# Kernel optimization log

Measured on AMD Instinct MI355X. Metric: run time of the kernel, lower is better.

Reference implementation:

```python
import jax, jax.numpy as jnp
import numpy as np

S, D = 16384, 1024


def setup_inputs() -> dict:
    key = jax.random.key(0)
    ks = jax.random.split(key, 7)
    stdv = 1.0 / np.sqrt(D)
    u = lambda k, shape: jax.random.uniform(k, shape, jnp.float32, -stdv, stdv)
    return {
        "x": jax.random.normal(ks[0], (S, D), jnp.float32),
        "Wq": u(ks[1], (D, D)), "bq": u(ks[2], (D,)),
        "Wk": u(ks[3], (D, D)), "bk": u(ks[4], (D,)),
        "Wv": u(ks[5], (D, D)), "bv": u(ks[6], (D,)),
    }


def reference(x, Wq, bq, Wk, bk, Wv, bv):
    # torch.nn.Linear: y = x @ W^T + b
    q = x @ Wq.T + bq          # [S, D]
    k = x @ Wk.T + bk          # [S, D]
    v = x @ Wv.T + bv          # [S, D]
    d = x.shape[-1]
    # NOTE: faithful to source -- scores are over the FEATURE axis: [D, D]
    scores = jnp.einsum('sd,se->de', q, k) / jnp.sqrt(jnp.float32(d))
    attn = jax.nn.softmax(scores, axis=-1)   # [D, D]
    out = v @ attn                           # [S, D]
    return out, attn
```

## Files before the change

### kernel.cpp

```cpp
#include <hip/hip_runtime.h>
#include <hip/hip_bf16.h>
#include <stdint.h>


#define S_ 16384
#define D_ 1024

typedef _Float16 half8 __attribute__((ext_vector_type(8)));
typedef _Float16 half4 __attribute__((ext_vector_type(4)));
typedef float f32x4 __attribute__((ext_vector_type(4)));

__device__ __forceinline__ void gload_lds16(const _Float16* g, _Float16* l) {
    __builtin_amdgcn_global_load_lds(
        (const __attribute__((address_space(1))) void*)g,
        (__attribute__((address_space(3))) void*)l, 16, 0, 0);
}

#define VM8() do { asm volatile("s_waitcnt vmcnt(8)" ::: "memory"); __builtin_amdgcn_sched_barrier(0); } while (0)
#define VM0() do { asm volatile("s_waitcnt vmcnt(0)" ::: "memory"); __builtin_amdgcn_sched_barrier(0); } while (0)
#define BAR() __builtin_amdgcn_s_barrier()
#define LGKM0() do { asm volatile("s_waitcnt lgkmcnt(0)" ::: "memory"); __builtin_amdgcn_sched_barrier(0); } while (0)
#define LGKM8() do { asm volatile("s_waitcnt lgkmcnt(8)" ::: "memory"); __builtin_amdgcn_sched_barrier(0); } while (0)
#define PRIO1() __builtin_amdgcn_s_setprio(1)
#define PRIO0() __builtin_amdgcn_s_setprio(0)

#define PAIR10(PI, BY, BX) do { \
    if ((PI) < 4) { BY = 0; BX = (PI); } \
    else if ((PI) < 7) { BY = 1; BX = (PI) - 3; } \
    else if ((PI) < 9) { BY = 2; BX = (PI) - 5; } \
    else { BY = 3; BX = 3; } \
} while (0)

#define STAGEA(H, KT, NX) do { \
    const _Float16* _s = srcA + (size_t)((H) * 128) * 16384 + (size_t)(KT) * 64; \
    _Float16* _d = AsS + (NX) * 16384 + ((H) * 128 + 8 * w) * 64; \
    gload_lds16(_s, _d); \
    gload_lds16(_s + (size_t)64 * 16384, _d + 4096); \
} while (0)

#define STAGEB(H, KT, NX) do { \
    const _Float16* _s = srcB + (size_t)((H) * 128) * 16384 + (size_t)(KT) * 64; \
    _Float16* _d = BsS + (NX) * 16384 + ((H) * 128 + 8 * w) * 64; \
    gload_lds16(_s, _d); \
    gload_lds16(_s + (size_t)64 * 16384, _d + 4096); \
} while (0)

#define READA(PA, QA) do { _Pragma("unroll") \
    for (int fm = 0; fm < 4; ++fm) { \
        af[fm][0] = *(const half8*)((PA) + (((QA) * 128 + fm * 16) << 7) + cx0); \
        af[fm][1] = *(const half8*)((PA) + (((QA) * 128 + fm * 16) << 7) + cx1); } \
} while (0)

#define READB(PB, BF, QB) do { _Pragma("unroll") \
    for (int fn = 0; fn < 2; ++fn) { \
        BF[fn][0] = *(const half8*)((PB) + (((QB) * 128 + fn * 16) << 7) + cx0); \
        BF[fn][1] = *(const half8*)((PB) + (((QB) * 128 + fn * 16) << 7) + cx1); } \
} while (0)

#define MFMAB(QA, QB, BF) do { _Pragma("unroll") \
    for (int fm = 0; fm < 4; ++fm) { _Pragma("unroll") \
        for (int fn = 0; fn < 2; ++fn) { \
            f32x4 _c = acc[(QA) * 4 + fm][(QB) * 2 + fn]; \
            _c = __builtin_amdgcn_mfma_f32_16x16x32_f16(af[fm][0], BF[fn][0], _c, 0, 0, 0); \
            _c = __builtin_amdgcn_mfma_f32_16x16x32_f16(af[fm][1], BF[fn][1], _c, 0, 0, 0); \
            acc[(QA) * 4 + fm][(QB) * 2 + fn] = _c; } } \
} while (0)

__global__ __launch_bounds__(512, 2)
void gemm256G(const _Float16* __restrict__ A, _Float16* __restrict__ C) {
    __shared__ _Float16 SM2[65536];
    _Float16* AsS = SM2;
    _Float16* BsS = SM2 + 32768;
    const int t = threadIdx.x;
    const int l = t & 63;
    const int w = t >> 6;
    const int wm = w >> 2, wn = w & 3;

    const int hb = blockIdx.x;
    const int lg = (hb & 7) * 20 + (hb >> 3);
    const int bz = lg / 10;
    const int pi = lg - bz * 10;
    int by, bx;
    PAIR10(pi, by, bx);
    const size_t m0 = (size_t)by * 256;
    const size_t n0 = (size_t)bx * 256;
    const size_t k0 = (size_t)bz * 1024;
    const long long coff = (long long)bz * 1048576LL;

    const int colsw = 8 * ((l & 7) ^ (l >> 3));
    const _Float16* srcA = A + (m0 + 8 * w + (l >> 3)) * (size_t)16384 + k0 + colsw;
    const _Float16* srcB = A + (n0 + 8 * w + (l >> 3)) * (size_t)16384 + k0 + colsw;

    const int cx0 = (((l >> 4) << 4)) ^ ((l & 7) << 4);
    const int cx1 = (64 + ((l >> 4) << 4)) ^ ((l & 7) << 4);
    const char* basePA = (const char*)AsS + ((wm * 64 + (l & 15)) << 7);
    const char* basePB = (const char*)BsS + ((wn * 32 + (l & 15)) << 7);

    f32x4 acc[8][4] = {};
    half8 af[4][2], bf0[2][2], bf1[2][2];

    const int nk = 16;

    STAGEA(0, 0, 0); STAGEB(0, 0, 0); STAGEB(1, 0, 0); STAGEA(1, 0, 0);
    STAGEA(0, 1, 1); STAGEB(0, 1, 1); STAGEB(1, 1, 1); STAGEA(1, 1, 1);

    for (int kt = 0; kt < nk; ++kt) {
        const int p = kt & 1;
        const int ks = kt + 2;
        const bool hs = ks < nk;
        const char* pA = basePA + p * 32768;
        const char* pB = basePB + p * 32768;

        if (kt == nk - 1) VM0(); else VM8();
        BAR();

        READA(pA, 0); READB(pB, bf0, 0);
        LGKM8();
        BAR(); LGKM0();
        PRIO1(); MFMAB(0, 0, bf0); PRIO0(); BAR();

        READB(pB, bf1, 1);
        if (hs) { STAGEA(0, ks, p); STAGEB(0, ks, p); }
        BAR(); LGKM0();
        PRIO1(); MFMAB(0, 1, bf1); PRIO0(); BAR();

        READA(pA, 1);
        if (hs) STAGEB(1, ks, p);
        BAR(); LGKM0();
        PRIO1(); MFMAB(1, 1, bf1); PRIO0(); BAR();

        if (hs) STAGEA(1, ks, p);
        PRIO1(); MFMAB(1, 0, bf0); PRIO0(); BAR();
    }

    _Float16* eb = SM2;
    const int cr = (l >> 4) << 2;
    const int cc = l & 15;
#pragma unroll
    for (int h = 0; h < 2; ++h) {
        BAR();
#pragma unroll
        for (int mm = 0; mm < 4; ++mm) {
#pragma unroll
            for (int n = 0; n < 4; ++n) {
                const int lrow0 = wm * 64 + mm * 16 + cr;
                const int lcol = (n >> 1) * 128 + wn * 32 + (n & 1) * 16 + cc;
#pragma unroll
                for (int r = 0; r < 4; ++r)
                    eb[(lrow0 + r) * 264 + lcol] = (_Float16)acc[h * 4 + mm][n][r];
            }
        }
        LGKM0();
        BAR();
#pragma unroll
        for (int i = 0; i < 8; ++i) {
            const int lrow = w * 16 + i * 2 + (l >> 5);
            const half8 v = *(const half8*)(eb + lrow * 264 + (l & 31) * 8);
            const size_t row = m0 + (size_t)h * 128 + lrow;
            const size_t col = n0 + (l & 31) * 8;
            __builtin_nontemporal_store(v,
                (half8*)(C + coff + (long long)row * 1024 + col));
        }
        LGKM0();
    }
}

__global__ __launch_bounds__(256)
void reduce_h_u(const _Float16* __restrict__ part, _Float16* __restrict__ G16) {
    const int b = blockIdx.x;
    const int ti = b >> 5;
    int by, bx;
    PAIR10(ti, by, bx);
    const int e0 = (b & 31) * 2048 + threadIdx.x * 8;
    const size_t row = (size_t)by * 256 + (e0 >> 8);
    const size_t col = (size_t)bx * 256 + (e0 & 255);
    const size_t off = row * 1024 + col;
    float s[8] = {};
    for (int z = 0; z < 16; ++z) {
        half8 v = *(const half8*)(part + (size_t)z * 1048576 + off);
#pragma unroll
        for (int j = 0; j < 8; ++j) s[j] += (float)v[j];
    }
    half8 o;
#pragma unroll
    for (int j = 0; j < 8; ++j) o[j] = (_Float16)s[j];
    *(half8*)(G16 + off) = o;
}

__global__ __launch_bounds__(256)
void mirror_g(_Float16* __restrict__ G) {
    __shared__ _Float16 tile[64][66];
    const int p = blockIdx.y;
    int by, bx;
    if (p < 3) { by = 0; bx = p + 1; }
    else if (p < 5) { by = 1; bx = p - 1; }
    else { by = 2; bx = 3; }
    const int sy = blockIdx.x >> 2, sx = blockIdx.x & 3;
    const int r0 = by * 256 + sy * 64;
    const int c0 = bx * 256 + sx * 64;
    const int t = threadIdx.x;
    const int cg = t & 15;
    const int rb = t >> 4;
#pragma unroll
    for (int it = 0; it < 4; ++it) {
        const int rr = rb + it * 16;
        half4 v = *(const half4*)(G + (size_t)(r0 + rr) * 1024 + c0 + cg * 4);
        tile[rr][cg * 4 + 0] = v[0]; tile[rr][cg * 4 + 1] = v[1];
        tile[rr][cg * 4 + 2] = v[2]; tile[rr][cg * 4 + 3] = v[3];
    }
    __syncthreads();
    const int i = t >> 2, ch = (t & 3) * 16;
    half8 h0v, h1v;
#pragma unroll
    for (int j = 0; j < 8; ++j) h0v[j] = tile[ch + j][i];
#pragma unroll
    for (int j = 0; j < 8; ++j) h1v[j] = tile[ch + 8 + j][i];
    *(half8*)(G + (size_t)(c0 + i) * 1024 + r0 + ch) = h0v;
    *(half8*)(G + (size_t)(c0 + i) * 1024 + r0 + ch + 8) = h1v;
}

#define STG128(SRC, LD, DST, KT) do { \
    const _Float16* _s = (SRC) + (size_t)(KT) * 64; \
    _Float16* _d = (DST) + 8 * w * 64; \
    gload_lds16(_s, _d); \
    gload_lds16(_s + (size_t)32 * (LD), _d + 2048); \
    gload_lds16(_s + (size_t)64 * (LD), _d + 4096); \
    gload_lds16(_s + (size_t)96 * (LD), _d + 6144); \
} while (0)

__global__ __launch_bounds__(256, 2)
void gemm128(const _Float16* __restrict__ A, const _Float16* __restrict__ B,
             float* __restrict__ C, const float* __restrict__ bias,
             int lda, int ldb, int ldc, int ksub,
             int ntx, int cpx) {
    __shared__ _Float16 SM[32768];
    const int t = threadIdx.x;
    const int l = t & 63;
    const int w = t >> 6;
    const int wm = w >> 1, wn = w & 1;

    const int hb = blockIdx.x;
    const int lg = (hb & 7) * cpx + (hb >> 3);
    const int by = lg / ntx;
    const int bx = lg - by * ntx;
    const size_t m0 = (size_t)by * 128;
    const size_t n0 = (size_t)bx * 128;

    const int colsw = 8 * ((l & 7) ^ (l >> 3));
    const _Float16* srcA = A + (m0 + 8 * w + (l >> 3)) * (size_t)lda + colsw;
    const _Float16* srcB = B + (n0 + 8 * w + (l >> 3)) * (size_t)ldb + colsw;

    const int cx0 = (((l >> 4) << 4)) ^ ((l & 7) << 4);
    const int cx1 = (64 + ((l >> 4) << 4)) ^ ((l & 7) << 4);
    const char* basePA = (const char*)SM + ((wm * 64 + (l & 15)) << 7);
    const char* basePB = (const char*)SM + 32768 + ((wn * 64 + (l & 15)) << 7);

    f32x4 acc[4][4] = {};
    half8 af[4][2], bf[4][2];

    const int nk = ksub >> 6;

    STG128(srcA, lda, SM + 0, 0);        STG128(srcB, ldb, SM + 16384, 0);
    STG128(srcA, lda, SM + 8192, 1);     STG128(srcB, ldb, SM + 24576, 1);

    for (int kt = 0; kt < nk; ++kt) {
        const int p = kt & 1;
        const int ks = kt + 2;
        const bool hs = ks < nk;
        const char* pA = basePA + p * 16384;
        const char* pB = basePB + p * 16384;

        if (kt == nk - 1) VM0(); else VM8();
        BAR();

#pragma unroll
        for (int fm = 0; fm < 4; ++fm) {
            af[fm][0] = *(const half8*)(pA + ((fm * 16) << 7) + cx0);
            af[fm][1] = *(const half8*)(pA + ((fm * 16) << 7) + cx1);
        }
#pragma unroll
        for (int fn = 0; fn < 4; ++fn) {
            bf[fn][0] = *(const half8*)(pB + ((fn * 16) << 7) + cx0);
            bf[fn][1] = *(const half8*)(pB + ((fn * 16) << 7) + cx1);
        }
        LGKM0();
        PRIO1();
#pragma unroll
        for (int fm = 0; fm < 4; ++fm)
#pragma unroll
            for (int fn = 0; fn < 4; ++fn)
                acc[fm][fn] = __builtin_amdgcn_mfma_f32_16x16x32_f16(af[fm][0], bf[fn][0], acc[fm][fn], 0, 0, 0);
        PRIO0();
        BAR();

        if (hs) {
            STG128(srcA, lda, SM + p * 8192, ks);
            STG128(srcB, ldb, SM + 16384 + p * 8192, ks);
        }
        PRIO1();
#pragma unroll
        for (int fm = 0; fm < 4; ++fm)
#pragma unroll
            for (int fn = 0; fn < 4; ++fn)
                acc[fm][fn] = __builtin_amdgcn_mfma_f32_16x16x32_f16(af[fm][1], bf[fn][1], acc[fm][fn], 0, 0, 0);
        PRIO0();
        BAR();
    }

    float* lw = (float*)((char*)SM + w * 16384);
    const int cr = (l >> 4) << 2;
    const int cc = l & 15;
    float bb4[4];
#pragma unroll
    for (int fn = 0; fn < 4; ++fn)
        bb4[fn] = bias[n0 + wn * 64 + fn * 16 + cc];
#pragma unroll
    for (int h = 0; h < 2; ++h) {
#pragma unroll
        for (int mm2 = 0; mm2 < 2; ++mm2) {
            const int mm = h * 2 + mm2;
#pragma unroll
            for (int fn = 0; fn < 4; ++fn) {
                const int lcol = fn * 16 + cc;
                const int lrow = mm2 * 16 + cr;
#pragma unroll
                for (int r = 0; r < 4; ++r)
                    lw[(lrow + r) * 68 + lcol] = acc[mm][fn][r] + bb4[fn];
            }
        }
        LGKM0();
        const size_t grow0 = m0 + (size_t)wm * 64 + h * 32;
#pragma unroll
        for (int i = 0; i < 8; ++i) {
            const int lrow = i * 4 + (l >> 4);
            const int lcol = (l & 15) * 4;
            const f32x4 v = *(const f32x4*)(lw + lrow * 68 + lcol);
            __builtin_nontemporal_store(v,
                (f32x4*)(C + (size_t)(grow0 + lrow) * ldc + n0 + wn * 64 + lcol));
        }
        LGKM0();
    }
}

template <int F16OUT>
__global__ __launch_bounds__(256, 2)
void gemm_s128(const _Float16* __restrict__ A, const _Float16* __restrict__ B,
               void* __restrict__ C, int lda, int ldb, int ldc, int ksub,
               long long mn) {
    __shared__ _Float16 SM[32768];
    const int t = threadIdx.x;
    const int l = t & 63;
    const int w = t >> 6;
    const int wm = w >> 1, wn = w & 1;

    const size_t m0 = (size_t)blockIdx.y * 128;
    const size_t n0 = (size_t)blockIdx.x * 128;
    const size_t k0 = (size_t)blockIdx.z * (size_t)ksub;
    const long long coff = (long long)blockIdx.z * mn;

    const int colsw = 8 * ((l & 7) ^ (l >> 3));
    const _Float16* srcA = A + (m0 + 8 * w + (l >> 3)) * (size_t)lda + k0 + colsw;
    const _Float16* srcB = B + (n0 + 8 * w + (l >> 3)) * (size_t)ldb + k0 + colsw;

    const int cx0 = (((l >> 4) << 4)) ^ ((l & 7) << 4);
    const int cx1 = (64 + ((l >> 4) << 4)) ^ ((l & 7) << 4);
    const char* basePA = (const char*)SM + ((wm * 64 + (l & 15)) << 7);
    const char* basePB = (const char*)SM + 32768 + ((wn * 64 + (l & 15)) << 7);

    f32x4 acc[4][4] = {};
    half8 af[4][2], bf[4][2];

    const int nk = ksub >> 6;

    STG128(srcA, lda, SM + 0, 0);        STG128(srcB, ldb, SM + 16384, 0);
    STG128(srcA, lda, SM + 8192, 1);     STG128(srcB, ldb, SM + 24576, 1);

    for (int kt = 0; kt < nk; ++kt) {
        const int p = kt & 1;
        const int ks = kt + 2;
        const bool hs = ks < nk;
        const char* pA = basePA + p * 16384;
        const char* pB = basePB + p * 16384;

        if (kt == nk - 1) VM0(); else VM8();
        BAR();

#pragma unroll
        for (int fm = 0; fm < 4; ++fm) {
            af[fm][0] = *(const half8*)(pA + ((fm * 16) << 7) + cx0);
            af[fm][1] = *(const half8*)(pA + ((fm * 16) << 7) + cx1);
        }
#pragma unroll
        for (int fn = 0; fn < 4; ++fn) {
            bf[fn][0] = *(const half8*)(pB + ((fn * 16) << 7) + cx0);
            bf[fn][1] = *(const half8*)(pB + ((fn * 16) << 7) + cx1);
        }
        LGKM0();
        PRIO1();
#pragma unroll
        for (int fm = 0; fm < 4; ++fm)
#pragma unroll
            for (int fn = 0; fn < 4; ++fn)
                acc[fm][fn] = __builtin_amdgcn_mfma_f32_16x16x32_f16(af[fm][0], bf[fn][0], acc[fm][fn], 0, 0, 0);
        PRIO0();
        BAR();

        if (hs) {
            STG128(srcA, lda, SM + p * 8192, ks);
            STG128(srcB, ldb, SM + 16384 + p * 8192, ks);
        }
        PRIO1();
#pragma unroll
        for (int fm = 0; fm < 4; ++fm)
#pragma unroll
            for (int fn = 0; fn < 4; ++fn)
                acc[fm][fn] = __builtin_amdgcn_mfma_f32_16x16x32_f16(af[fm][1], bf[fn][1], acc[fm][fn], 0, 0, 0);
        PRIO0();
        BAR();
    }

    const int cr = (l >> 4) << 2;
    const int cc = l & 15;

    if (F16OUT) {
        _Float16* eb = SM;
#pragma unroll
        for (int fm = 0; fm < 4; ++fm) {
#pragma unroll
            for (int fn = 0; fn < 4; ++fn) {
                const int lrow0 = wm * 64 + fm * 16 + cr;
                const int lcol = wn * 64 + fn * 16 + cc;
#pragma unroll
                for (int r = 0; r < 4; ++r)
                    eb[(lrow0 + r) * 132 + lcol] = (_Float16)acc[fm][fn][r];
            }
        }
        LGKM0();
        BAR();
        _Float16* Ch = (_Float16*)C;
#pragma unroll
        for (int i = 0; i < 8; ++i) {
            const int row = i * 16 + (t >> 4);
            const int colh = (t & 15) * 8;
            const half8 v = *(const half8*)(eb + row * 132 + colh);
            *(half8*)(Ch + coff + (long long)(m0 + row) * ldc + n0 + colh) = v;
        }
    } else {
        float* lw = (float*)((char*)SM + w * 16384);
        float* Cf = (float*)C;
#pragma unroll
        for (int h = 0; h < 2; ++h) {
#pragma unroll
            for (int mm2 = 0; mm2 < 2; ++mm2) {
                const int mm = h * 2 + mm2;
#pragma unroll
                for (int fn = 0; fn < 4; ++fn) {
                    const int lcol = fn * 16 + cc;
                    const int lrow = mm2 * 16 + cr;
#pragma unroll
                    for (int r = 0; r < 4; ++r)
                        lw[(lrow + r) * 68 + lcol] = acc[mm][fn][r];
                }
            }
            LGKM0();
            const size_t grow0 = m0 + (size_t)wm * 64 + h * 32;
#pragma unroll
            for (int i = 0; i < 8; ++i) {
                const int lrow = i * 4 + (l >> 4);
                const int lcol = (l & 15) * 4;
                const f32x4 v = *(const f32x4*)(lw + lrow * 68 + lcol);
                *(f32x4*)(Cf + coff + (long long)(grow0 + lrow) * ldc + n0 + wn * 64 + lcol) = v;
            }
            LGKM0();
        }
    }
}

template <int WRITE_ROW, int COLSUM>
__global__ __launch_bounds__(256)
void cast_transpose(const float* __restrict__ in, _Float16* __restrict__ outRow,
                    _Float16* __restrict__ outT, float* __restrict__ msum, int ldT) {
    __shared__ _Float16 tile[64][66];
    __shared__ float red[16][16][4];
    const int t = threadIdx.x;
    const int c0 = blockIdx.x * 64;
    const int r0 = blockIdx.y * 64;
    const int cg = t & 15;
    const int rb = t >> 4;
    f32x4 csum = {};
#pragma unroll
    for (int it = 0; it < 4; ++it) {
        const int rr = rb + it * 16;
        f32x4 v = *(const f32x4*)(in + (size_t)(r0 + rr) * 1024 + c0 + cg * 4);
        if (COLSUM) { csum[0] += v[0]; csum[1] += v[1]; csum[2] += v[2]; csum[3] += v[3]; }
        _Float16 h0 = (_Float16)v[0], h1 = (_Float16)v[1];
        _Float16 h2 = (_Float16)v[2], h3 = (_Float16)v[3];
        tile[rr][cg * 4 + 0] = h0; tile[rr][cg * 4 + 1] = h1;
        tile[rr][cg * 4 + 2] = h2; tile[rr][cg * 4 + 3] = h3;
        if (WRITE_ROW) {
            half4 h = {h0, h1, h2, h3};
            *(half4*)(outRow + (size_t)(r0 + rr) * 1024 + c0 + cg * 4) = h;
        }
    }
    if (COLSUM) {
        red[rb][cg][0] = csum[0]; red[rb][cg][1] = csum[1];
        red[rb][cg][2] = csum[2]; red[rb][cg][3] = csum[3];
    }
    __syncthreads();
    if (COLSUM && t < 64) {
        float s = 0.f;
#pragma unroll
        for (int k = 0; k < 16; ++k) s += red[k][t >> 2][t & 3];
        atomicAdd(msum + c0 + t, s);
    }
    const int i = t >> 2, ch = (t & 3) * 16;
    half8 h0v, h1v;
#pragma unroll
    for (int j = 0; j < 8; ++j) h0v[j] = tile[ch + j][i];
#pragma unroll
    for (int j = 0; j < 8; ++j) h1v[j] = tile[ch + 8 + j][i];
    *(half8*)(outT + (size_t)(c0 + i) * ldT + r0 + ch) = h0v;
    *(half8*)(outT + (size_t)(c0 + i) * ldT + r0 + ch + 8) = h1v;
}

__global__ __launch_bounds__(256)
void prep_w(const float* __restrict__ Wq, const float* __restrict__ Wk,
            const float* __restrict__ Wv, const float* __restrict__ bq,
            const float* __restrict__ m,
            _Float16* __restrict__ wq16, _Float16* __restrict__ wk16,
            _Float16* __restrict__ wvT16,
            float* __restrict__ u2, float* __restrict__ w) {
    __shared__ _Float16 tile[64][66];
    __shared__ float wred[4];
    const int b = blockIdx.x;
    const int t = threadIdx.x;

    if (b < 1024) {
        const bool isQ = b < 512;
        const int bb = isQ ? b : b - 512;
        const float* W = isQ ? Wq : Wk;
        _Float16* o = isQ ? wq16 : wk16;
        const size_t base = (size_t)bb * 2048 + (size_t)t * 8;
        const f32x4* p = (const f32x4*)(W + base);
        f32x4 x0 = p[0], x1 = p[1];
        half8 h;
        h[0] = (_Float16)x0[0]; h[1] = (_Float16)x0[1];
        h[2] = (_Float16)x0[2]; h[3] = (_Float16)x0[3];
        h[4] = (_Float16)x1[0]; h[5] = (_Float16)x1[1];
        h[6] = (_Float16)x1[2]; h[7] = (_Float16)x1[3];
        ((half8*)o)[bb * 256 + t] = h;
        const int col = (t * 8) & 1023;
        f32x4 m0 = *(const f32x4*)(m + col);
        f32x4 m1 = *(const f32x4*)(m + col + 4);
        float s = x0[0] * m0[0] + x0[1] * m0[1] + x0[2] * m0[2] + x0[3] * m0[3]
                + x1[0] * m1[0] + x1[1] * m1[1] + x1[2] * m1[2] + x1[3] * m1[3];
        for (int o2 = 32; o2; o2 >>= 1) s += __shfl_xor(s, o2);
        if ((t & 63) == 0) wred[t >> 6] = s;
        __syncthreads();
        if (t == 0) {
            const int rA = 2 * bb, rB = 2 * bb + 1;
            const float vA = wred[0] + wred[1];
            const float vB = wred[2] + wred[3];
            if (isQ) {
                u2[rA] = vA + 16384.0f * bq[rA];
                u2[rB] = vB + 16384.0f * bq[rB];
            } else {
                w[rA] = vA;
                w[rB] = vB;
            }
        }
        return;
    }

    const int bb = b - 1024;
    const int c0 = (bb & 15) * 64;
    const int r0 = (bb >> 4) * 64;
    const int cg = t & 15;
    const int rb = t >> 4;
#pragma unroll
    for (int it = 0; it < 4; ++it) {
        const int rr = rb + it * 16;
        f32x4 v = *(const f32x4*)(Wv + (size_t)(r0 + rr) * 1024 + c0 + cg * 4);
        tile[rr][cg * 4 + 0] = (_Float16)v[0];
        tile[rr][cg * 4 + 1] = (_Float16)v[1];
        tile[rr][cg * 4 + 2] = (_Float16)v[2];
        tile[rr][cg * 4 + 3] = (_Float16)v[3];
    }
    __syncthreads();
    const int i = t >> 2, ch = (t & 3) * 16;
    half8 h0v, h1v;
#pragma unroll
    for (int j = 0; j < 8; ++j) h0v[j] = tile[ch + j][i];
#pragma unroll
    for (int j = 0; j < 8; ++j) h1v[j] = tile[ch + 8 + j][i];
    *(half8*)(wvT16 + (size_t)(c0 + i) * 1024 + r0 + ch) = h0v;
    *(half8*)(wvT16 + (size_t)(c0 + i) * 1024 + r0 + ch + 8) = h1v;
}

__global__ void zero_vec(float* __restrict__ p, int n) {
    int i = blockIdx.x * 256 + threadIdx.x;
    if (i < n) p[i] = 0.f;
}

__global__ __launch_bounds__(256)
void reduce_h(const _Float16* __restrict__ part, _Float16* __restrict__ outh,
              int nz) {
    const size_t off = ((size_t)blockIdx.x * 256 + threadIdx.x) * 8;
    float s[8] = {};
    for (int z = 0; z < nz; ++z) {
        half8 v = *(const half8*)(part + (size_t)z * 1048576 + off);
#pragma unroll
        for (int j = 0; j < 8; ++j) s[j] += (float)v[j];
    }
    half8 o;
#pragma unroll
    for (int j = 0; j < 8; ++j) o[j] = (_Float16)s[j];
    *(half8*)(outh + off) = o;
}

__global__ __launch_bounds__(256)
void softmax_rows(const float* __restrict__ part, const float* __restrict__ u2,
                  const float* __restrict__ bq, const float* __restrict__ bk,
                  const float* __restrict__ w,
                  float* __restrict__ P, _Float16* __restrict__ PT) {
    const int a = blockIdx.x;
    const int t = threadIdx.x;
    __shared__ float red[8];
    const size_t off = (size_t)a * 1024 + t * 4;
    f32x4 s = {};
#pragma unroll
    for (int z = 0; z < 4; ++z) {
        f32x4 v = *(const f32x4*)(part + (size_t)z * 1048576 + off);
        s[0] += v[0]; s[1] += v[1]; s[2] += v[2]; s[3] += v[3];
    }
    const float ru = u2[a], rb = bq[a];
    f32x4 bk4 = *(const f32x4*)(bk + t * 4);
    f32x4 w4 = *(const f32x4*)(w + t * 4);
#pragma unroll
    for (int j = 0; j < 4; ++j) s[j] = (s[j] + ru * bk4[j] + rb * w4[j]) * 0.03125f;

    float m = fmaxf(fmaxf(s[0], s[1]), fmaxf(s[2], s[3]));
    for (int o = 32; o; o >>= 1) m = fmaxf(m, __shfl_xor(m, o));
    if ((t & 63) == 0) red[t >> 6] = m;
    __syncthreads();
    m = fmaxf(fmaxf(red[0], red[1]), fmaxf(red[2], red[3]));

    float e0 = expf(s[0] - m), e1 = expf(s[1] - m);
    float e2 = expf(s[2] - m), e3 = expf(s[3] - m);
    float sum = e0 + e1 + e2 + e3;
    for (int o = 32; o; o >>= 1) sum += __shfl_xor(sum, o);
    if ((t & 63) == 0) red[4 + (t >> 6)] = sum;
    __syncthreads();
    sum = red[4] + red[5] + red[6] + red[7];
    const float inv = 1.0f / sum;

    f32x4 o4 = {e0 * inv, e1 * inv, e2 * inv, e3 * inv};
    *(f32x4*)(P + off) = o4;
    const int b = t * 4;
    PT[(size_t)(b + 0) * 1024 + a] = (_Float16)o4[0];
    PT[(size_t)(b + 1) * 1024 + a] = (_Float16)o4[1];
    PT[(size_t)(b + 2) * 1024 + a] = (_Float16)o4[2];
    PT[(size_t)(b + 3) * 1024 + a] = (_Float16)o4[3];
}

__global__ __launch_bounds__(256)
void attn_bv(const float* __restrict__ attn, const float* __restrict__ bv,
             float* __restrict__ c) {
    const int j = blockIdx.x * 256 + threadIdx.x;
    const int a0 = blockIdx.y * 64;
    float s = 0.f;
#pragma unroll 4
    for (int k = 0; k < 64; ++k) {
        const int a = a0 + k;
        s += attn[(size_t)a * 1024 + j] * bv[a];
    }
    atomicAdd(c + j, s);
}

extern "C" void kernel_launch(void* const* d_in, const int* in_sizes, int n_in,
                              void* d_out, int out_size, void* d_ws, size_t ws_size,
                              hipStream_t stream) {
    const float* x  = (const float*)d_in[0];
    const float* Wq = (const float*)d_in[1];
    const float* bq = (const float*)d_in[2];
    const float* Wk = (const float*)d_in[3];
    const float* bk = (const float*)d_in[4];
    const float* Wv = (const float*)d_in[5];
    const float* bv = (const float*)d_in[6];
    float* out  = (float*)d_out;
    float* attn = out + (size_t)S_ * D_;

    char* ws = (char*)d_ws;
    float*    part  = (float*)ws;
    _Float16* partH = (_Float16*)ws;
    _Float16* x16   = (_Float16*)(ws + 33554432);
    _Float16* xT16  = (_Float16*)(ws + 67108864);
    _Float16* wq16  = (_Float16*)(ws + 100663296);
    _Float16* wk16  = (_Float16*)(ws + 102760448);
    _Float16* wvT16 = (_Float16*)(ws + 104857600);
    _Float16* G16   = (_Float16*)(ws + 106954752);
    _Float16* U16   = (_Float16*)(ws + 109051904);
    _Float16* PT    = (_Float16*)(ws + 111149056);
    _Float16* MT16  = (_Float16*)(ws + 113246208);
    float*    mvec  = (float*)(ws + 115343360);
    float*    u2    = mvec + 1024;
    float*    wv    = u2 + 1024;
    float*    cvec  = wv + 1024;

    zero_vec<<<16, 256, 0, stream>>>(mvec, 4096);
    cast_transpose<1, 1><<<dim3(16, 256), 256, 0, stream>>>(x, x16, xT16, mvec, S_);
    prep_w<<<1280, 256, 0, stream>>>(Wq, Wk, Wv, bq, mvec,
                                     wq16, wk16, wvT16, u2, wv);

    gemm256G<<<160, 512, 0, stream>>>(xT16, partH);
    reduce_h_u<<<320, 256, 0, stream>>>(partH, G16);
    mirror_g<<<dim3(16, 6), 256, 0, stream>>>(G16);
    gemm_s128<1><<<dim3(8, 8, 4), 256, 0, stream>>>(wq16, G16, (void*)partH,
                                                    1024, 1024, 1024, 256, 1048576);
    reduce_h<<<512, 256, 0, stream>>>(partH, U16, 4);
    gemm_s128<0><<<dim3(8, 8, 4), 256, 0, stream>>>(U16, wk16, (void*)part,
                                                    1024, 1024, 1024, 256, 1048576);
    softmax_rows<<<1024, 256, 0, stream>>>(part, u2, bq, bk, wv, attn, PT);
    attn_bv<<<dim3(4, 16), 256, 0, stream>>>(attn, bv, cvec);
    gemm_s128<1><<<dim3(8, 8, 4), 256, 0, stream>>>(PT, wvT16, (void*)partH,
                                                    1024, 1024, 1024, 256, 1048576);
    reduce_h<<<512, 256, 0, stream>>>(partH, MT16, 4);
    gemm128<<<1024, 256, 0, stream>>>(x16, MT16, out, cvec,
                                      1024, 1024, 1024, 1024, 8, 128);
}
```

Baseline: 165.5 us.

## Fuse weight prep into Gram GEMM, mirror in reduce, bias-vec into MT GEMM

Weight casting and transposing now run as extra blocks inside the Gram GEMM launch instead of as a separate prep kernel. The Gram reduction writes the mirrored transpose of off-diagonal tiles itself, which removes the mirror_g kernel. The attn·bv vector reduction now runs as extra blocks of a dedicated PT×WvT GEMM kernel. Together these cut three kernel launches and the serial gaps between them, at the cost of mixed-role blocks competing for CUs and the heavier 512-thread LDS footprint being applied to the lightweight prep blocks.

New measurement: 154.9 us, median of 2. 1.07x faster.

```diff
diff --git a/kernel.cpp b/kernel.cpp
--- a/kernel.cpp
+++ b/kernel.cpp
@@ -67,111 +67,197 @@
 } while (0)
 
 __global__ __launch_bounds__(512, 2)
-void gemm256G(const _Float16* __restrict__ A, _Float16* __restrict__ C) {
+void g_and_prep(const _Float16* __restrict__ A, _Float16* __restrict__ C,
+                const float* __restrict__ Wq, const float* __restrict__ Wk,
+                const float* __restrict__ Wv, const float* __restrict__ bq,
+                const float* __restrict__ m,
+                _Float16* __restrict__ wq16, _Float16* __restrict__ wk16,
+                _Float16* __restrict__ wvT16,
+                float* __restrict__ u2, float* __restrict__ wvec) {
     __shared__ _Float16 SM2[65536];
-    _Float16* AsS = SM2;
-    _Float16* BsS = SM2 + 32768;
     const int t = threadIdx.x;
-    const int l = t & 63;
-    const int w = t >> 6;
-    const int wm = w >> 2, wn = w & 3;
-
-    const int hb = blockIdx.x;
-    const int lg = (hb & 7) * 20 + (hb >> 3);
-    const int bz = lg / 10;
-    const int pi = lg - bz * 10;
-    int by, bx;
-    PAIR10(pi, by, bx);
-    const size_t m0 = (size_t)by * 256;
-    const size_t n0 = (size_t)bx * 256;
-    const size_t k0 = (size_t)bz * 1024;
-    const long long coff = (long long)bz * 1048576LL;
-
-    const int colsw = 8 * ((l & 7) ^ (l >> 3));
-    const _Float16* srcA = A + (m0 + 8 * w + (l >> 3)) * (size_t)16384 + k0 + colsw;
-    const _Float16* srcB = A + (n0 + 8 * w + (l >> 3)) * (size_t)16384 + k0 + colsw;
-
-    const int cx0 = (((l >> 4) << 4)) ^ ((l & 7) << 4);
-    const int cx1 = (64 + ((l >> 4) << 4)) ^ ((l & 7) << 4);
-    const char* basePA = (const char*)AsS + ((wm * 64 + (l & 15)) << 7);
-    const char* basePB = (const char*)BsS + ((wn * 32 + (l & 15)) << 7);
-
-    f32x4 acc[8][4] = {};
-    half8 af[4][2], bf0[2][2], bf1[2][2];
-
-    const int nk = 16;
-
-    STAGEA(0, 0, 0); STAGEB(0, 0, 0); STAGEB(1, 0, 0); STAGEA(1, 0, 0);
-    STAGEA(0, 1, 1); STAGEB(0, 1, 1); STAGEB(1, 1, 1); STAGEA(1, 1, 1);
-
-    for (int kt = 0; kt < nk; ++kt) {
-        const int p = kt & 1;
-        const int ks = kt + 2;
-        const bool hs = ks < nk;
-        const char* pA = basePA + p * 32768;
-        const char* pB = basePB + p * 32768;
-
-        if (kt == nk - 1) VM0(); else VM8();
-        BAR();
-
-        READA(pA, 0); READB(pB, bf0, 0);
-        LGKM8();
-        BAR(); LGKM0();
-        PRIO1(); MFMAB(0, 0, bf0); PRIO0(); BAR();
-
-        READB(pB, bf1, 1);
-        if (hs) { STAGEA(0, ks, p); STAGEB(0, ks, p); }
-        BAR(); LGKM0();
-        PRIO1(); MFMAB(0, 1, bf1); PRIO0(); BAR();
-
-        READA(pA, 1);
-        if (hs) STAGEB(1, ks, p);
-        BAR(); LGKM0();
-        PRIO1(); MFMAB(1, 1, bf1); PRIO0(); BAR();
-
-        if (hs) STAGEA(1, ks, p);
-        PRIO1(); MFMAB(1, 0, bf0); PRIO0(); BAR();
-    }
-
-    _Float16* eb = SM2;
-    const int cr = (l >> 4) << 2;
-    const int cc = l & 15;
-#pragma unroll
-    for (int h = 0; h < 2; ++h) {
-        BAR();
-#pragma unroll
-        for (int mm = 0; mm < 4; ++mm) {
-#pragma unroll
-            for (int n = 0; n < 4; ++n) {
-                const int lrow0 = wm * 64 + mm * 16 + cr;
-                const int lcol = (n >> 1) * 128 + wn * 32 + (n & 1) * 16 + cc;
-#pragma unroll
-                for (int r = 0; r < 4; ++r)
-                    eb[(lrow0 + r) * 264 + lcol] = (_Float16)acc[h * 4 + mm][n][r];
+
+    if (blockIdx.x < 160) {
+        _Float16* AsS = SM2;
+        _Float16* BsS = SM2 + 32768;
+        const int l = t & 63;
+        const int w = t >> 6;
+        const int wm = w >> 2, wn = w & 3;
+
+        const int hb = blockIdx.x;
+        const int lg = (hb & 7) * 20 + (hb >> 3);
+        const int bz = lg / 10;
+        const int pi = lg - bz * 10;
+        int by, bx;
+        PAIR10(pi, by, bx);
+        const size_t m0 = (size_t)by * 256;
+        const size_t n0 = (size_t)bx * 256;
+        const size_t k0 = (size_t)bz * 1024;
+        const long long coff = (long long)bz * 1048576LL;
+
+        const int colsw = 8 * ((l & 7) ^ (l >> 3));
+        const _Float16* srcA = A + (m0 + 8 * w + (l >> 3)) * (size_t)16384 + k0 + colsw;
+        const _Float16* srcB = A + (n0 + 8 * w + (l >> 3)) * (size_t)16384 + k0 + colsw;
+
+        const int cx0 = (((l >> 4) << 4)) ^ ((l & 7) << 4);
+        const int cx1 = (64 + ((l >> 4) << 4)) ^ ((l & 7) << 4);
+        const char* basePA = (const char*)AsS + ((wm * 64 + (l & 15)) << 7);
+        const char* basePB = (const char*)BsS + ((wn * 32 + (l & 15)) << 7);
+
+        f32x4 acc[8][4] = {};
+        half8 af[4][2], bf0[2][2], bf1[2][2];
+
+        const int nk = 16;
+
+        STAGEA(0, 0, 0); STAGEB(0, 0, 0); STAGEB(1, 0, 0); STAGEA(1, 0, 0);
+        STAGEA(0, 1, 1); STAGEB(0, 1, 1); STAGEB(1, 1, 1); STAGEA(1, 1, 1);
+
+        for (int kt = 0; kt < nk; ++kt) {
+            const int p = kt & 1;
+            const int ks = kt + 2;
+            const bool hs = ks < nk;
+            const char* pA = basePA + p * 32768;
+            const char* pB = basePB + p * 32768;
+
+            if (kt == nk - 1) VM0(); else VM8();
+            BAR();
+
+            READA(pA, 0); READB(pB, bf0, 0);
+            LGKM8();
+            BAR(); LGKM0();
+            PRIO1(); MFMAB(0, 0, bf0); PRIO0(); BAR();
+
+            READB(pB, bf1, 1);
+            if (hs) { STAGEA(0, ks, p); STAGEB(0, ks, p); }
+            BAR(); LGKM0();
+            PRIO1(); MFMAB(0, 1, bf1); PRIO0(); BAR();
+
+            READA(pA, 1);
+            if (hs) STAGEB(1, ks, p);
+            BAR(); LGKM0();
+            PRIO1(); MFMAB(1, 1, bf1); PRIO0(); BAR();
+
+            if (hs) STAGEA(1, ks, p);
+            PRIO1(); MFMAB(1, 0, bf0); PRIO0(); BAR();
+        }
+
+        _Float16* eb = SM2;
+        const int cr = (l >> 4) << 2;
+        const int cc = l & 15;
+#pragma unroll
+        for (int h = 0; h < 2; ++h) {
+            BAR();
+#pragma unroll
+            for (int mm = 0; mm < 4; ++mm) {
+#pragma unroll
+                for (int n = 0; n < 4; ++n) {
+                    const int lrow0 = wm * 64 + mm * 16 + cr;
+                    const int lcol = (n >> 1) * 128 + wn * 32 + (n & 1) * 16 + cc;
+#pragma unroll
+                    for (int r = 0; r < 4; ++r)
+                        eb[(lrow0 + r) * 264 + lcol] = (_Float16)acc[h * 4 + mm][n][r];
+                }
             }
-        }
-        LGKM0();
-        BAR();
-#pragma unroll
-        for (int i = 0; i < 8; ++i) {
-            const int lrow = w * 16 + i * 2 + (l >> 5);
-            const half8 v = *(const half8*)(eb + lrow * 264 + (l & 31) * 8);
-            const size_t row = m0 + (size_t)h * 128 + lrow;
-            const size_t col = n0 + (l & 31) * 8;
-            __builtin_nontemporal_store(v,
-                (half8*)(C + coff + (long long)row * 1024 + col));
-        }
-        LGKM0();
+            LGKM0();
+            BAR();
+#pragma unroll
+            for (int i = 0; i < 8; ++i) {
+                const int lrow = w * 16 + i * 2 + (l >> 5);
+                const half8 v = *(const half8*)(eb + lrow * 264 + (l & 31) * 8);
+                const size_t row = m0 + (size_t)h * 128 + lrow;
+                const size_t col = n0 + (l & 31) * 8;
+                __builtin_nontemporal_store(v,
+                    (half8*)(C + coff + (long long)row * 1024 + col));
+            }
+            LGKM0();
+        }
+        return;
+    }
+
+    const int h = t >> 8;
+    const int vt = t & 255;
+    const int vb = (blockIdx.x - 160) * 2 + h;
+    _Float16* tileh = SM2 + h * 4224;
+    float* wredAll = (float*)(SM2 + 16896);
+    const bool isW = vb < 1024;
+
+    if (isW) {
+        const bool isQ = vb < 512;
+        const int bb = isQ ? vb : vb - 512;
+        const float* W = isQ ? Wq : Wk;
+        _Float16* o = isQ ? wq16 : wk16;
+        const size_t base = (size_t)bb * 2048 + (size_t)vt * 8;
+        const f32x4* p = (const f32x4*)(W + base);
+        f32x4 x0 = p[0], x1 = p[1];
+        half8 hv;
+        hv[0] = (_Float16)x0[0]; hv[1] = (_Float16)x0[1];
+        hv[2] = (_Float16)x0[2]; hv[3] = (_Float16)x0[3];
+        hv[4] = (_Float16)x1[0]; hv[5] = (_Float16)x1[1];
+        hv[6] = (_Float16)x1[2]; hv[7] = (_Float16)x1[3];
+        ((half8*)o)[bb * 256 + vt] = hv;
+        const int col = (vt * 8) & 1023;
+        f32x4 m0v = *(const f32x4*)(m + col);
+        f32x4 m1v = *(const f32x4*)(m + col + 4);
+        float s = x0[0] * m0v[0] + x0[1] * m0v[1] + x0[2] * m0v[2] + x0[3] * m0v[3]
+                + x1[0] * m1v[0] + x1[1] * m1v[1] + x1[2] * m1v[2] + x1[3] * m1v[3];
+        for (int o2 = 32; o2; o2 >>= 1) s += __shfl_xor(s, o2);
+        if ((t & 63) == 0) wredAll[t >> 6] = s;
+    } else {
+        const int bb = vb - 1024;
+        const int c0 = (bb & 15) * 64;
+        const int r0 = (bb >> 4) * 64;
+        const int cg = vt & 15;
+        const int rb = vt >> 4;
+#pragma unroll
+        for (int it = 0; it < 4; ++it) {
+            const int rr = rb + it * 16;
+            f32x4 v = *(const f32x4*)(Wv + (size_t)(r0 + rr) * 1024 + c0 + cg * 4);
+            tileh[rr * 66 + cg * 4 + 0] = (_Float16)v[0];
+            tileh[rr * 66 + cg * 4 + 1] = (_Float16)v[1];
+            tileh[rr * 66 + cg * 4 + 2] = (_Float16)v[2];
+            tileh[rr * 66 + cg * 4 + 3] = (_Float16)v[3];
+        }
+    }
+    __syncthreads();
+    if (isW) {
+        if (vt == 0) {
+            const bool isQ = vb < 512;
+            const int bb = isQ ? vb : vb - 512;
+            const int rA = 2 * bb, rB = 2 * bb + 1;
+            const float vA = wredAll[h * 4 + 0] + wredAll[h * 4 + 1];
+            const float vB = wredAll[h * 4 + 2] + wredAll[h * 4 + 3];
+            if (isQ) {
+                u2[rA] = vA + 16384.0f * bq[rA];
+                u2[rB] = vB + 16384.0f * bq[rB];
+            } else {
+                wvec[rA] = vA;
+                wvec[rB] = vB;
+            }
+        }
+    } else {
+        const int bb = vb - 1024;
+        const int c0 = (bb & 15) * 64;
+        const int r0 = (bb >> 4) * 64;
+        const int i = vt >> 2, ch = (vt & 3) * 16;
+        half8 h0v, h1v;
+#pragma unroll
+        for (int j = 0; j < 8; ++j) h0v[j] = tileh[(ch + j) * 66 + i];
+#pragma unroll
+        for (int j = 0; j < 8; ++j) h1v[j] = tileh[(ch + 8 + j) * 66 + i];
+        *(half8*)(wvT16 + (size_t)(c0 + i) * 1024 + r0 + ch) = h0v;
+        *(half8*)(wvT16 + (size_t)(c0 + i) * 1024 + r0 + ch + 8) = h1v;
     }
 }
 
 __global__ __launch_bounds__(256)
 void reduce_h_u(const _Float16* __restrict__ part, _Float16* __restrict__ G16) {
+    __shared__ _Float16 lt[256][9];
     const int b = blockIdx.x;
     const int ti = b >> 5;
     int by, bx;
     PAIR10(ti, by, bx);
-    const int e0 = (b & 31) * 2048 + threadIdx.x * 8;
+    const int t = threadIdx.x;
+    const int e0 = (b & 31) * 2048 + t * 8;
     const size_t row = (size_t)by * 256 + (e0 >> 8);
     const size_t col = (size_t)bx * 256 + (e0 & 255);
     const size_t off = row * 1024 + col;
@@ -185,38 +271,19 @@
 #pragma unroll
     for (int j = 0; j < 8; ++j) o[j] = (_Float16)s[j];
     *(half8*)(G16 + off) = o;
-}
-
-__global__ __launch_bounds__(256)
-void mirror_g(_Float16* __restrict__ G) {
-    __shared__ _Float16 tile[64][66];
-    const int p = blockIdx.y;
-    int by, bx;
-    if (p < 3) { by = 0; bx = p + 1; }
-    else if (p < 5) { by = 1; bx = p - 1; }
-    else { by = 2; bx = 3; }
-    const int sy = blockIdx.x >> 2, sx = blockIdx.x & 3;
-    const int r0 = by * 256 + sy * 64;
-    const int c0 = bx * 256 + sx * 64;
-    const int t = threadIdx.x;
-    const int cg = t & 15;
-    const int rb = t >> 4;
-#pragma unroll
-    for (int it = 0; it < 4; ++it) {
-        const int rr = rb + it * 16;
-        half4 v = *(const half4*)(G + (size_t)(r0 + rr) * 1024 + c0 + cg * 4);
-        tile[rr][cg * 4 + 0] = v[0]; tile[rr][cg * 4 + 1] = v[1];
-        tile[rr][cg * 4 + 2] = v[2]; tile[rr][cg * 4 + 3] = v[3];
+
+    const bool offd = (by != bx);
+    if (offd) {
+        const int cl = (t & 31) * 8;
+        const int rl = t >> 5;
+#pragma unroll
+        for (int j = 0; j < 8; ++j) lt[cl + j][rl] = o[j];
     }
     __syncthreads();
-    const int i = t >> 2, ch = (t & 3) * 16;
-    half8 h0v, h1v;
-#pragma unroll
-    for (int j = 0; j < 8; ++j) h0v[j] = tile[ch + j][i];
-#pragma unroll
-    for (int j = 0; j < 8; ++j) h1v[j] = tile[ch + 8 + j][i];
-    *(half8*)(G + (size_t)(c0 + i) * 1024 + r0 + ch) = h0v;
-    *(half8*)(G + (size_t)(c0 + i) * 1024 + r0 + ch + 8) = h1v;
+    if (offd) {
+        half8 v = *(const half8*)(&lt[t][0]);
+        *(half8*)(G16 + ((size_t)(bx * 256 + t)) * 1024 + by * 256 + (b & 31) * 8) = v;
+    }
 }
 
 #define STG128(SRC, LD, DST, KT) do { \
@@ -473,6 +540,124 @@
             }
             LGKM0();
         }
+    }
+}
+
+__global__ __launch_bounds__(256, 2)
+void gemm_mt_bv(const _Float16* __restrict__ A, const _Float16* __restrict__ B,
+                _Float16* __restrict__ Cp,
+                const float* __restrict__ attn, const float* __restrict__ bv,
+                float* __restrict__ cvec) {
+    const int idx = blockIdx.x;
+    if (idx >= 256) {
+        const int bb = idx - 256;
+        const int j = (bb & 3) * 256 + threadIdx.x;
+        const int a0 = (bb >> 2) * 64;
+        float s = 0.f;
+#pragma unroll 4
+        for (int k = 0; k < 64; ++k) {
+            const int a = a0 + k;
+            s += attn[(size_t)a * 1024 + j] * bv[a];
+        }
+        atomicAdd(cvec + j, s);
+        return;
+    }
+
+    __shared__ _Float16 SM[32768];
+    const int t = threadIdx.x;
+    const int l = t & 63;
+    const int w = t >> 6;
+    const int wm = w >> 1, wn = w & 1;
+
+    const int bx = idx & 7, by = (idx >> 3) & 7, bz = idx >> 6;
+    const size_t m0 = (size_t)by * 128;
+    const size_t n0 = (size_t)bx * 128;
+    const size_t k0 = (size_t)bz * 256;
+    const long long coff = (long long)bz * 1048576LL;
+
+    const int colsw = 8 * ((l & 7) ^ (l >> 3));
+    const _Float16* srcA = A + (m0 + 8 * w + (l >> 3)) * (size_t)1024 + k0 + colsw;
+    const _Float16* srcB = B + (n0 + 8 * w + (l >> 3)) * (size_t)1024 + k0 + colsw;
+
+    const int cx0 = (((l >> 4) << 4)) ^ ((l & 7) << 4);
+    const int cx1 = (64 + ((l >> 4) << 4)) ^ ((l & 7) << 4);
+    const char* basePA = (const char*)SM + ((wm * 64 + (l & 15)) << 7);
+    const char* basePB = (const char*)SM + 32768 + ((wn * 64 + (l & 15)) << 7);
+
+    f32x4 acc[4][4] = {};
+    half8 af[4][2], bf[4][2];
+
+    const int nk = 4;
+
+    STG128(srcA, 1024, SM + 0, 0);        STG128(srcB, 1024, SM + 16384, 0);
+    STG128(srcA, 1024, SM + 8192, 1);     STG128(srcB, 1024, SM + 24576, 1);
+
+    for (int kt = 0; kt < nk; ++kt) {
+        const int p = kt & 1;
+        const int ks = kt + 2;
+        const bool hs = ks < nk;
+        const char* pA = basePA + p * 16384;
+        const char* pB = basePB + p * 16384;
+
+        if (kt == nk - 1) VM0(); else VM8();
+        BAR();
+
+#pragma unroll
+        for (int fm = 0; fm < 4; ++fm) {
+            af[fm][0] = *(const half8*)(pA + ((fm * 16) << 7) + cx0);
+            af[fm][1] = *(const half8*)(pA + ((fm * 16) << 7) + cx1);
+        }
+#pragma unroll
+        for (int fn = 0; fn < 4; ++fn) {
+            bf[fn][0] = *(const half8*)(pB + ((fn * 16) << 7) + cx0);
+            bf[fn][1] = *(const half8*)(pB + ((fn * 16) << 7) + cx1);
+        }
+        LGKM0();
+        PRIO1();
+#pragma unroll
+        for (int fm = 0; fm < 4; ++fm)
+#pragma unroll
+            for (int fn = 0; fn < 4; ++fn)
+                acc[fm][fn] = __builtin_amdgcn_mfma_f32_16x16x32_f16(af[fm][0], bf[fn][0], acc[fm][fn], 0, 0, 0);
+        PRIO0();
+        BAR();
+
+        if (hs) {
+            STG128(srcA, 1024, SM + p * 8192, ks);
+            STG128(srcB, 1024, SM + 16384 + p * 8192, ks);
+        }
+        PRIO1();
+#pragma unroll
+        for (int fm = 0; fm < 4; ++fm)
+#pragma unroll
+            for (int fn = 0; fn < 4; ++fn)
+                acc[fm][fn] = __builtin_amdgcn_mfma_f32_16x16x32_f16(af[fm][1], bf[fn][1], acc[fm][fn], 0, 0, 0);
+        PRIO0();
+        BAR();
+    }
+
+    const int cr = (l >> 4) << 2;
+    const int cc = l & 15;
+    _Float16* eb = SM;
+#pragma unroll
+    for (int fm = 0; fm < 4; ++fm) {
+#pragma unroll
+        for (int fn = 0; fn < 4; ++fn) {
+            const int lrow0 = wm * 64 + fm * 16 + cr;
+            const int lcol = wn * 64 + fn * 16 + cc;
+#pragma unroll
+            for (int r = 0; r < 4; ++r)
+                eb[(lrow0 + r) * 132 + lcol] = (_Float16)acc[fm][fn][r];
+        }
+    }
+    LGKM0();
+    BAR();
+#pragma unroll
+    for (int i = 0; i < 8; ++i) {
+        const int row = i * 16 + (t >> 4);
+        const int colh = (t & 15) * 8;
+        const half8 v = *(const half8*)(eb + row * 132 + colh);
+        *(half8*)(Cp + coff + (long long)(m0 + row) * 1024 + n0 + colh) = v;
     }
 }
 
@@ -523,80 +708,6 @@
     *(half8*)(outT + (size_t)(c0 + i) * ldT + r0 + ch + 8) = h1v;
 }
 
-__global__ __launch_bounds__(256)
-void prep_w(const float* __restrict__ Wq, const float* __restrict__ Wk,
-            const float* __restrict__ Wv, const float* __restrict__ bq,
-            const float* __restrict__ m,
-            _Float16* __restrict__ wq16, _Float16* __restrict__ wk16,
-            _Float16* __restrict__ wvT16,
-            float* __restrict__ u2, float* __restrict__ w) {
-    __shared__ _Float16 tile[64][66];
-    __shared__ float wred[4];
-    const int b = blockIdx.x;
-    const int t = threadIdx.x;
-
-    if (b < 1024) {
-        const bool isQ = b < 512;
-        const int bb = isQ ? b : b - 512;
-        const float* W = isQ ? Wq : Wk;
-        _Float16* o = isQ ? wq16 : wk16;
-        const size_t base = (size_t)bb * 2048 + (size_t)t * 8;
-        const f32x4* p = (const f32x4*)(W + base);
-        f32x4 x0 = p[0], x1 = p[1];
-        half8 h;
-        h[0] = (_Float16)x0[0]; h[1] = (_Float16)x0[1];
-        h[2] = (_Float16)x0[2]; h[3] = (_Float16)x0[3];
-        h[4] = (_Float16)x1[0]; h[5] = (_Float16)x1[1];
-        h[6] = (_Float16)x1[2]; h[7] = (_Float16)x1[3];
-        ((half8*)o)[bb * 256 + t] = h;
-        const int col = (t * 8) & 1023;
-        f32x4 m0 = *(const f32x4*)(m + col);
-        f32x4 m1 = *(const f32x4*)(m + col + 4);
-        float s = x0[0] * m0[0] + x0[1] * m0[1] + x0[2] * m0[2] + x0[3] * m0[3]
-                + x1[0] * m1[0] + x1[1] * m1[1] + x1[2] * m1[2] + x1[3] * m1[3];
-        for (int o2 = 32; o2; o2 >>= 1) s += __shfl_xor(s, o2);
-        if ((t & 63) == 0) wred[t >> 6] = s;
-        __syncthreads();
-        if (t == 0) {
-            const int rA = 2 * bb, rB = 2 * bb + 1;
-            const float vA = wred[0] + wred[1];
-            const float vB = wred[2] + wred[3];
-            if (isQ) {
-                u2[rA] = vA + 16384.0f * bq[rA];
-                u2[rB] = vB + 16384.0f * bq[rB];
-            } else {
-                w[rA] = vA;
-                w[rB] = vB;
-            }
-        }
-        return;
-    }
-
-    const int bb = b - 1024;
-    const int c0 = (bb & 15) * 64;
-    const int r0 = (bb >> 4) * 64;
-    const int cg = t & 15;
-    const int rb = t >> 4;
-#pragma unroll
-    for (int it = 0; it < 4; ++it) {
-        const int rr = rb + it * 16;
-        f32x4 v = *(const f32x4*)(Wv + (size_t)(r0 + rr) * 1024 + c0 + cg * 4);
-        tile[rr][cg * 4 + 0] = (_Float16)v[0];
-        tile[rr][cg * 4 + 1] = (_Float16)v[1];
-        tile[rr][cg * 4 + 2] = (_Float16)v[2];
-        tile[rr][cg * 4 + 3] = (_Float16)v[3];
-    }
-    __syncthreads();
-    const int i = t >> 2, ch = (t & 3) * 16;
-    half8 h0v, h1v;
-#pragma unroll
-    for (int j = 0; j < 8; ++j) h0v[j] = tile[ch + j][i];
-#pragma unroll
-    for (int j = 0; j < 8; ++j) h1v[j] = tile[ch + 8 + j][i];
-    *(half8*)(wvT16 + (size_t)(c0 + i) * 1024 + r0 + ch) = h0v;
-    *(half8*)(wvT16 + (size_t)(c0 + i) * 1024 + r0 + ch + 8) = h1v;
-}
-
 __global__ void zero_vec(float* __restrict__ p, int n) {
     int i = blockIdx.x * 256 + threadIdx.x;
     if (i < n) p[i] = 0.f;
@@ -661,20 +772,6 @@
     PT[(size_t)(b + 1) * 1024 + a] = (_Float16)o4[1];
     PT[(size_t)(b + 2) * 1024 + a] = (_Float16)o4[2];
     PT[(size_t)(b + 3) * 1024 + a] = (_Float16)o4[3];
-}
-
-__global__ __launch_bounds__(256)
-void attn_bv(const float* __restrict__ attn, const float* __restrict__ bv,
-             float* __restrict__ c) {
-    const int j = blockIdx.x * 256 + threadIdx.x;
-    const int a0 = blockIdx.y * 64;
-    float s = 0.f;
-#pragma unroll 4
-    for (int k = 0; k < 64; ++k) {
-        const int a = a0 + k;
-        s += attn[(size_t)a * 1024 + j] * bv[a];
-    }
-    atomicAdd(c + j, s);
 }
 
 extern "C" void kernel_launch(void* const* d_in, const int* in_sizes, int n_in,
@@ -709,21 +806,17 @@
 
     zero_vec<<<16, 256, 0, stream>>>(mvec, 4096);
     cast_transpose<1, 1><<<dim3(16, 256), 256, 0, stream>>>(x, x16, xT16, mvec, S_);
-    prep_w<<<1280, 256, 0, stream>>>(Wq, Wk, Wv, bq, mvec,
-                                     wq16, wk16, wvT16, u2, wv);
-
-    gemm256G<<<160, 512, 0, stream>>>(xT16, partH);
+
+    g_and_prep<<<800, 512, 0, stream>>>(xT16, partH, Wq, Wk, Wv, bq, mvec,
+                                        wq16, wk16, wvT16, u2, wv);
     reduce_h_u<<<320, 256, 0, stream>>>(partH, G16);
-    mirror_g<<<dim3(16, 6), 256, 0, stream>>>(G16);
     gemm_s128<1><<<dim3(8, 8, 4), 256, 0, stream>>>(wq16, G16, (void*)partH,
                                                     1024, 1024, 1024, 256, 1048576);
     reduce_h<<<512, 256, 0, stream>>>(partH, U16, 4);
     gemm_s128<0><<<dim3(8, 8, 4), 256, 0, stream>>>(U16, wk16, (void*)part,
                                                     1024, 1024, 1024, 256, 1048576);
     softmax_rows<<<1024, 256, 0, stream>>>(part, u2, bq, bk, wv, attn, PT);
-    attn_bv<<<dim3(4, 16), 256, 0, stream>>>(attn, bv, cvec);
-    gemm_s128<1><<<dim3(8, 8, 4), 256, 0, stream>>>(PT, wvT16, (void*)partH,
-                                                    1024, 1024, 1024, 256, 1048576);
+    gemm_mt_bv<<<320, 256, 0, stream>>>(PT, wvT16, partH, attn, bv, cvec);
     reduce_h<<<512, 256, 0, stream>>>(partH, MT16, 4);
     gemm128<<<1024, 256, 0, stream>>>(x16, MT16, out, cvec,
                                       1024, 1024, 1024, 1024, 8, 128);
```
